# Kernel tuning notes

Hardware: AMD Instinct MI355X
Metric: run time of the kernel (lower is better)

## Reference

```python
import jax, jax.numpy as jnp
import numpy as np

EPS_BN = 1e-5
EPS_LN = 1e-5

def _bn(x, g, b, m, v):
    # inference-mode BatchNorm2d over channel dim 1
    scale = g / jnp.sqrt(v + EPS_BN)
    return x * scale[None, :, None, None] + (b - m * scale)[None, :, None, None]

def _conv1x1(x, w, b=None):
    y = jnp.einsum('bchw,oc->bohw', x, w)
    if b is not None:
        y = y + b[None, :, None, None]
    return y

def _gelu(x):
    return jax.nn.gelu(x, approximate=False)

def setup_inputs() -> dict:
    key = jax.random.key(0)
    ks = jax.random.split(key, 40)
    B, C, H, W = 32, 160, 56, 56
    C5, C3 = C // 5, C * 3
    s = 0.05
    d = {}
    d['x'] = jax.random.normal(ks[0], (B, C, H, W), jnp.float32)
    d['bn1_g'] = jax.random.uniform(ks[1], (C,), jnp.float32, 0.5, 1.5)
    d['bn1_b'] = jax.random.normal(ks[2], (C,)) * s
    d['bn1_m'] = jax.random.normal(ks[3], (C,)) * s
    d['bn1_v'] = jnp.ones((C,), jnp.float32)
    names = ['t', 'b', 'r', 'l', 'c']
    for i, n in enumerate(names):
        d['w' + n] = jax.random.normal(ks[4 + i], (C5, C)) * s
        d['b' + n] = jax.random.normal(ks[9 + i], (C5,)) * s
    d['wf1'] = jax.random.normal(ks[14], (C, C)) * s
    d['bf1'] = jax.random.normal(ks[15], (C,)) * s
    d['bn2_g'] = jax.random.uniform(ks[16], (C,), jnp.float32, 0.5, 1.5)
    d['bn2_b'] = jax.random.normal(ks[17], (C,)) * s
    d['bn2_m'] = jax.random.normal(ks[18], (C,)) * s
    d['bn2_v'] = jnp.ones((C,), jnp.float32)
    d['wph'] = jax.random.normal(ks[19], (W, W)) * s
    d['bph'] = jax.random.normal(ks[20], (W,)) * s
    d['wpw'] = jax.random.normal(ks[21], (H, H)) * s
    d['bpw'] = jax.random.normal(ks[22], (H,)) * s
    d['wf2'] = jax.random.normal(ks[23], (C, C3)) * s
    d['ln_g'] = jax.random.uniform(ks[24], (C,), jnp.float32, 0.5, 1.5)
    d['ln_b'] = jax.random.normal(ks[25], (C,)) * s
    d['wfc1'] = jax.random.normal(ks[26], (C3, C)) * s
    d['bfc1'] = jax.random.normal(ks[27], (C3,)) * s
    d['wfc2'] = jax.random.normal(ks[28], (C, C3)) * s
    d['bfc2'] = jax.random.normal(ks[29], (C,)) * s
    d['step'] = 1
    return d

def reference(x, bn1_g, bn1_b, bn1_m, bn1_v, wt, bt, wb, bb, wr, br, wl, bl, wc, bc,
              wf1, bf1, bn2_g, bn2_b, bn2_m, bn2_v, wph, bph, wpw, bpw, wf2,
              ln_g, ln_b, wfc1, bfc1, wfc2, bfc2, step):
    B, C, H, W = x.shape
    # ---- localMix: ShiftedPillarsConcatentation_BNAct_NP5 ----
    h = _gelu(_bn(x, bn1_g, bn1_b, bn1_m, bn1_v))
    x_t = _conv1x1(h, wt, bt)
    x_b = _conv1x1(h, wb, bb)
    x_r = _conv1x1(h, wr, br)
    x_l = _conv1x1(h, wl, bl)
    x_c = _conv1x1(h, wc, bc)
    # pad then narrow exactly as torch: t/l shift by 1, b/r shift by step
    x_t = jnp.pad(x_t, ((0, 0), (0, 0), (0, step), (0, 0)))[:, :, 1:1 + H, :]
    x_b = jnp.pad(x_b, ((0, 0), (0, 0), (step, 0), (0, 0)))[:, :, 0:H, :]
    x_l = jnp.pad(x_l, ((0, 0), (0, 0), (0, 0), (0, step)))[:, :, :, 1:1 + W]
    x_r = jnp.pad(x_r, ((0, 0), (0, 0), (0, 0), (step, 0)))[:, :, :, 0:W]
    lm = _conv1x1(jnp.concatenate([x_t, x_b, x_r, x_l, x_c], axis=1), wf1, bf1)
    # ---- globalMix: sparseMLP_BNAct ----
    g = _gelu(_bn(lm, bn2_g, bn2_b, bn2_m, bn2_v))
    # proj_h mixes the W axis (input permuted to (B,W,C,H)), bias per output W
    x_h = jnp.einsum('bchw,vw->bchv', g, wph) + bph[None, None, None, :]
    # proj_w mixes the H axis (input permuted to (B,H,C,W)), bias per output H
    x_w = jnp.einsum('bchw,uh->bcuw', g, wpw) + bpw[None, None, :, None]
    gm = _conv1x1(jnp.concatenate([g, x_h, x_w], axis=1), wf2)  # no bias
    x1 = gm + x  # residual 1
    # ---- channelMix: LN + Mlp over channels ----
    y = jnp.transpose(x1, (0, 2, 3, 1))  # BHWC
    mu = jnp.mean(y, axis=-1, keepdims=True)
    var = jnp.mean(jnp.square(y - mu), axis=-1, keepdims=True)
    y = (y - mu) / jnp.sqrt(var + EPS_LN) * ln_g + ln_b
    y = _gelu(jnp.einsum('bhwc,fc->bhwf', y, wfc1) + bfc1)
    y = jnp.einsum('bhwf,cf->bhwc', y, wfc2) + bfc2
    return jnp.transpose(y, (0, 3, 1, 2)) + x1  # residual 2
```

## Files before the change

### kernel.cpp

```cpp
#include <hip/hip_runtime.h>
#include <hip/hip_bf16.h>
#include <math.h>

typedef __hip_bfloat16 bf16;
typedef __attribute__((ext_vector_type(8))) short s8v;
typedef __attribute__((ext_vector_type(4))) float f4v;

#define Bn  32
#define Cn  160
#define HWn 3136
#define Pn  100352

__device__ __forceinline__ float b2f(bf16 v){ return __bfloat162float(v); }
__device__ __forceinline__ bf16  f2b(float v){ return __float2bfloat16(v); }
__device__ __forceinline__ float bits2f(unsigned short u){
    union { float f; unsigned int i; } x; x.i = ((unsigned int)u) << 16; return x.f;
}
__device__ __forceinline__ float gelu_f(float x){ return 0.5f*x*(1.0f + erff(x*0.7071067811865476f)); }

#define MFMA(a,b,c) __builtin_amdgcn_mfma_f32_16x16x32_bf16((a),(b),(c),0,0,0)

__global__ __launch_bounds__(256) void k0_prep(
    const float* __restrict__ wt, const float* __restrict__ wb_, const float* __restrict__ wr,
    const float* __restrict__ wl, const float* __restrict__ wc,
    const float* __restrict__ bt, const float* __restrict__ bb_, const float* __restrict__ br,
    const float* __restrict__ bl, const float* __restrict__ bc,
    const float* __restrict__ wf1, const float* __restrict__ bf1,
    const float* __restrict__ g2, const float* __restrict__ b2, const float* __restrict__ m2, const float* __restrict__ v2,
    const float* __restrict__ wf2, const float* __restrict__ wfc1, const float* __restrict__ wfc2,
    const float* __restrict__ wph, const float* __restrict__ wpw,
    bf16* wcat, bf16* wf1b, bf16* wf2b, bf16* wfc1b, bf16* wfc2b, bf16* wphb, bf16* wpwb,
    float* bcat, float* epsv, float* eptv)
{
    int idx = blockIdx.x*256 + threadIdx.x;
    if (idx < 25600){ int o = idx/160, k = idx - o*160; int gi = o>>5, oo = o&31;
        const float* wp = gi==0?wt: gi==1?wb_: gi==2?wr: gi==3?wl: wc;
        wcat[idx] = f2b(wp[oo*160+k]); return; }
    idx -= 25600;
    if (idx < 25600){ wf1b[idx] = f2b(wf1[idx]); return; }
    idx -= 25600;
    if (idx < 76800){ wf2b[idx] = f2b(wf2[idx]); return; }
    idx -= 76800;
    if (idx < 76800){ wfc1b[idx] = f2b(wfc1[idx]); return; }
    idx -= 76800;
    if (idx < 76800){ wfc2b[idx] = f2b(wfc2[idx]); return; }
    idx -= 76800;
    if (idx < 4096){ int v = idx>>6, w = idx&63;
        wphb[idx] = (v<56 && w<56) ? f2b(wph[v*56+w]) : f2b(0.f); return; }
    idx -= 4096;
    if (idx < 4096){ int v = idx>>6, w = idx&63;
        wpwb[idx] = (v<56 && w<56) ? f2b(wpw[v*56+w]) : f2b(0.f); return; }
    idx -= 4096;
    if (idx < 160){ int o = idx; int gi = o>>5, oo = o&31;
        const float* bp = gi==0?bt: gi==1?bb_: gi==2?br: gi==3?bl: bc;
        bcat[o] = bp[oo]; return; }
    idx -= 160;
    if (idx < 160){ int o = idx; float s = g2[o]*rsqrtf(v2[o]+1e-5f);
        epsv[o] = s; eptv[o] = (bf1[o]-m2[o])*s + b2[o]; return; }
}

__global__ __launch_bounds__(256) void k1_bn_gelu_tr(const float* __restrict__ x,
    const float* __restrict__ g, const float* __restrict__ b,
    const float* __restrict__ m, const float* __restrict__ v,
    bf16* __restrict__ hT)
{
    __shared__ float tile[64*161];
    __shared__ float sc[160], sh[160];
    int blk = blockIdx.x; int bb = blk/49; int hw0 = (blk - bb*49)*64;
    int tid = threadIdx.x;
    if (tid < 160){
        float s = g[tid] * rsqrtf(v[tid] + 1e-5f);
        sc[tid] = s; sh[tid] = b[tid] - m[tid]*s;
    }
    __syncthreads();
    const float* xb = x + (size_t)bb*Cn*HWn + hw0;
    for (int idx = tid; idx < 160*64; idx += 256){
        int c = idx >> 6, p = idx & 63;
        float val = xb[(size_t)c*HWn + p];
        tile[p*161 + c] = gelu_f(val*sc[c] + sh[c]);
    }
    __syncthreads();
    bf16* ho = hT + ((size_t)bb*HWn + hw0)*Cn;
    for (int idx = tid; idx < 64*160; idx += 256){
        int p = idx/160, c = idx - p*160;
        ho[idx] = f2b(tile[p*161 + c]);
    }
}

__global__ __launch_bounds__(256) void k2_conv5(const bf16* __restrict__ hT,
    const bf16* __restrict__ wcat, const float* __restrict__ bcat, bf16* __restrict__ y5T)
{
    __shared__ __align__(16) unsigned short Bs[2][16*168];
    int tid = threadIdx.x, wave = tid>>6, lane = tid&63, m = lane&15, q = lane>>4;
    size_t pos0 = (size_t)blockIdx.x*64;
    const unsigned short* Ap = (const unsigned short*)hT + (pos0 + wave*16 + m)*160 + q*8;
    s8v a[5];
    #pragma unroll
    for (int kb = 0; kb < 5; ++kb) a[kb] = *(const s8v*)(Ap + kb*32);
    { const s8v* sp = (const s8v*)((const unsigned short*)wcat);
      for (int c = tid; c < 320; c += 256){ int row = c/20, col = (c - row*20)*8;
          *(s8v*)&Bs[0][row*168 + col] = sp[c]; } }
    __syncthreads();
    for (int s = 0; s < 10; ++s){
        if (s+1 < 10){
            const s8v* sp = (const s8v*)((const unsigned short*)wcat + (size_t)(s+1)*2560);
            for (int c = tid; c < 320; c += 256){ int row = c/20, col = (c - row*20)*8;
                *(s8v*)&Bs[(s+1)&1][row*168 + col] = sp[c]; }
        }
        f4v acc = {0.f,0.f,0.f,0.f};
        const unsigned short* Bp = &Bs[s&1][m*168 + q*8];
        #pragma unroll
        for (int kb = 0; kb < 5; ++kb) acc = MFMA(a[kb], *(const s8v*)(Bp + kb*32), acc);
        float bias = bcat[s*16 + m];
        bf16* yo = y5T + (pos0 + wave*16 + q*4)*160 + s*16 + m;
        #pragma unroll
        for (int r = 0; r < 4; ++r) yo[r*160] = f2b(acc[r] + bias);
        __syncthreads();
    }
}

__global__ __launch_bounds__(256) void k3_wf1(const bf16* __restrict__ y5T,
    const bf16* __restrict__ wf1b, const float* __restrict__ epsv, const float* __restrict__ eptv,
    bf16* __restrict__ gT)
{
    __shared__ __align__(16) unsigned short Bs[2][16*168];
    int tid = threadIdx.x, wave = tid>>6, lane = tid&63, m = lane&15, q = lane>>4;
    int blk = blockIdx.x; int bb = blk/49; int hw0 = (blk - bb*49)*64;
    size_t pos0 = (size_t)bb*HWn + hw0;
    int phw = hw0 + wave*16 + m; int h = phw/56, w = phw - h*56;
    s8v a[5];
    #pragma unroll
    for (int kb = 0; kb < 5; ++kb){
        int h2 = h, w2 = w; bool ok = true;
        if      (kb == 0){ h2 = h+1; ok = (h2 < 56); }
        else if (kb == 1){ h2 = h-1; ok = (h2 >= 0); }
        else if (kb == 2){ w2 = w-1; ok = (w2 >= 0); }
        else if (kb == 3){ w2 = w+1; ok = (w2 < 56); }
        if (ok){
            const unsigned short* Ap = (const unsigned short*)y5T +
                ((size_t)bb*HWn + h2*56 + w2)*160 + kb*32 + q*8;
            a[kb] = *(const s8v*)Ap;
        } else {
            a[kb] = (s8v){0,0,0,0,0,0,0,0};
        }
    }
    { const s8v* sp = (const s8v*)((const unsigned short*)wf1b);
      for (int c = tid; c < 320; c += 256){ int row = c/20, col = (c - row*20)*8;
          *(s8v*)&Bs[0][row*168 + col] = sp[c]; } }
    __syncthreads();
    for (int s = 0; s < 10; ++s){
        if (s+1 < 10){
            const s8v* sp = (const s8v*)((const unsigned short*)wf1b + (size_t)(s+1)*2560);
            for (int c = tid; c < 320; c += 256){ int row = c/20, col = (c - row*20)*8;
                *(s8v*)&Bs[(s+1)&1][row*168 + col] = sp[c]; }
        }
        f4v acc = {0.f,0.f,0.f,0.f};
        const unsigned short* Bp = &Bs[s&1][m*168 + q*8];
        #pragma unroll
        for (int kb = 0; kb < 5; ++kb) acc = MFMA(a[kb], *(const s8v*)(Bp + kb*32), acc);
        int o = s*16 + m;
        float es = epsv[o], et = eptv[o];
        bf16* go = gT + (pos0 + wave*16 + q*4)*160 + o;
        #pragma unroll
        for (int r = 0; r < 4; ++r) go[r*160] = f2b(gelu_f(acc[r]*es + et));
        __syncthreads();
    }
}

__global__ __launch_bounds__(256) void k4_projh(const bf16* __restrict__ gT,
    const bf16* __restrict__ wphb, const float* __restrict__ bph, bf16* __restrict__ xhT)
{
    __shared__ __align__(16) unsigned short gS[160*72];
    int tid = threadIdx.x, wave = tid>>6, lane = tid&63, m = lane&15, q = lane>>4;
    int blk = blockIdx.x; int b = blk/56, h = blk - b*56;
    const unsigned short* ga = (const unsigned short*)gT + ((size_t)b*HWn + h*56)*160;
    for (int idx = tid; idx < 56*160; idx += 256){
        int w = idx/160, c = idx - w*160;
        gS[c*72 + w] = ga[idx];
    }
    for (int idx = tid; idx < 160*8; idx += 256){
        int c = idx>>3, w = 56 + (idx&7);
        gS[c*72 + w] = 0;
    }
    __syncthreads();
    int v0 = wave*16;
    s8v a[2];
    #pragma unroll
    for (int kb = 0; kb < 2; ++kb)
        a[kb] = *(const s8v*)((const unsigned short*)wphb + (v0+m)*64 + kb*32 + q*8);
    int v = v0 + q*4;
    for (int s = 0; s < 10; ++s){
        f4v acc = {0.f,0.f,0.f,0.f};
        const unsigned short* Bp = &gS[(s*16+m)*72 + q*8];
        #pragma unroll
        for (int kb = 0; kb < 2; ++kb) acc = MFMA(a[kb], *(const s8v*)(Bp + kb*32), acc);
        #pragma unroll
        for (int r = 0; r < 4; ++r){
            int vv = v + r;
            if (vv < 56)
                xhT[((size_t)b*HWn + h*56 + vv)*160 + s*16 + m] = f2b(acc[r] + bph[vv]);
        }
    }
}

__global__ __launch_bounds__(256) void k5_projw(const bf16* __restrict__ gT,
    const bf16* __restrict__ wpwb, const float* __restrict__ bpw, bf16* __restrict__ xwT)
{
    __shared__ __align__(16) unsigned short gS[160*72];
    int tid = threadIdx.x, wave = tid>>6, lane = tid&63, m = lane&15, q = lane>>4;
    int blk = blockIdx.x; int b = blk/56, w = blk - b*56;
    const unsigned short* gbase = (const unsigned short*)gT + ((size_t)b*HWn + w)*160;
    for (int idx = tid; idx < 56*160; idx += 256){
        int hh = idx/160, c = idx - hh*160;
        gS[c*72 + hh] = gbase[(size_t)hh*56*160 + c];
    }
    for (int idx = tid; idx < 160*8; idx += 256){
        int c = idx>>3, hh = 56 + (idx&7);
        gS[c*72 + hh] = 0;
    }
    __syncthreads();
    int v0 = wave*16;
    s8v a[2];
    #pragma unroll
    for (int kb = 0; kb < 2; ++kb)
        a[kb] = *(const s8v*)((const unsigned short*)wpwb + (v0+m)*64 + kb*32 + q*8);
    int v = v0 + q*4;
    for (int s = 0; s < 10; ++s){
        f4v acc = {0.f,0.f,0.f,0.f};
        const unsigned short* Bp = &gS[(s*16+m)*72 + q*8];
        #pragma unroll
        for (int kb = 0; kb < 2; ++kb) acc = MFMA(a[kb], *(const s8v*)(Bp + kb*32), acc);
        #pragma unroll
        for (int r = 0; r < 4; ++r){
            int vv = v + r;
            if (vv < 56)
                xwT[((size_t)b*HWn + vv*56 + w)*160 + s*16 + m] = f2b(acc[r] + bpw[vv]);
        }
    }
}

__global__ __launch_bounds__(256) void k6_wf2(const bf16* __restrict__ gT,
    const bf16* __restrict__ xhT, const bf16* __restrict__ xwT,
    const bf16* __restrict__ wf2b, bf16* __restrict__ gm)
{
    __shared__ __align__(16) unsigned short Bs[2][16*488];
    int tid = threadIdx.x, wave = tid>>6, lane = tid&63, m = lane&15, q = lane>>4;
    size_t pos0 = (size_t)blockIdx.x*64;
    size_t prow = (pos0 + wave*16 + m)*160;
    s8v a[15];
    #pragma unroll
    for (int kb = 0; kb < 15; ++kb){
        const bf16* src = (kb < 5) ? gT : (kb < 10 ? xhT : xwT);
        int kc = (kb - (kb < 5 ? 0 : (kb < 10 ? 5 : 10)))*32 + q*8;
        a[kb] = *(const s8v*)((const unsigned short*)src + prow + kc);
    }
    { const s8v* sp = (const s8v*)((const unsigned short*)wf2b);
      for (int c = tid; c < 960; c += 256){ int row = c/60, col = (c - row*60)*8;
          *(s8v*)&Bs[0][row*488 + col] = sp[c]; } }
    __syncthreads();
    for (int s = 0; s < 10; ++s){
        if (s+1 < 10){
            const s8v* sp = (const s8v*)((const unsigned short*)wf2b + (size_t)(s+1)*7680);
            for (int c = tid; c < 960; c += 256){ int row = c/60, col = (c - row*60)*8;
                *(s8v*)&Bs[(s+1)&1][row*488 + col] = sp[c]; }
        }
        f4v acc = {0.f,0.f,0.f,0.f};
        const unsigned short* Bp = &Bs[s&1][m*488 + q*8];
        #pragma unroll
        for (int kb = 0; kb < 15; ++kb) acc = MFMA(a[kb], *(const s8v*)(Bp + kb*32), acc);
        bf16* go = gm + (pos0 + wave*16 + q*4)*160 + s*16 + m;
        #pragma unroll
        for (int r = 0; r < 4; ++r) go[r*160] = f2b(acc[r]);
        __syncthreads();
    }
}

__global__ __launch_bounds__(256) void k7_ln_fc1(const float* __restrict__ x,
    const bf16* __restrict__ gm,
    const float* __restrict__ lng, const float* __restrict__ lnb,
    const bf16* __restrict__ wfc1b, const float* __restrict__ bfc1, bf16* __restrict__ u)
{
    __shared__ float Xs[64*161];
    __shared__ __align__(16) unsigned short As[64*168];
    __shared__ __align__(16) unsigned short Bs[2][16*168];
    int tid = threadIdx.x, wave = tid>>6, lane = tid&63, m = lane&15, q = lane>>4;
    int blk = blockIdx.x; int bb = blk/49; int hw0 = (blk - bb*49)*64;
    size_t pos0 = (size_t)bb*HWn + hw0;
    const float* xb = x + (size_t)bb*Cn*HWn + hw0;
    for (int idx = tid; idx < 160*64; idx += 256){
        int o = idx >> 6, p = idx & 63;
        Xs[p*161 + o] = xb[(size_t)o*HWn + p];
    }
    { const s8v* sp = (const s8v*)((const unsigned short*)wfc1b);
      for (int c = tid; c < 320; c += 256){ int row = c/20, col = (c - row*20)*8;
          *(s8v*)&Bs[0][row*168 + col] = sp[c]; } }
    __syncthreads();
    {
        int p = tid >> 2, q4 = tid & 3;
        const unsigned short* gp = (const unsigned short*)gm + (pos0 + p)*160 + q4*40;
        float s = 0.f, ss = 0.f;
        #pragma unroll 8
        for (int i = 0; i < 40; ++i){
            int c = q4*40 + i;
            float vv = Xs[p*161 + c] + bits2f(gp[i]);
            Xs[p*161 + c] = vv;
            s += vv; ss += vv*vv;
        }
        s  += __shfl_xor(s, 1);  ss += __shfl_xor(ss, 1);
        s  += __shfl_xor(s, 2);  ss += __shfl_xor(ss, 2);
        float mean = s * (1.f/160.f);
        float var  = ss * (1.f/160.f) - mean*mean;
        float rstd = rsqrtf(var + 1e-5f);
        #pragma unroll 8
        for (int i = 0; i < 40; ++i){
            int c = q4*40 + i;
            float nv = (Xs[p*161 + c] - mean)*rstd*lng[c] + lnb[c];
            union { unsigned short us; bf16 b; } cv; cv.b = f2b(nv);
            As[p*168 + c] = cv.us;
        }
    }
    __syncthreads();
    s8v a[5];
    const unsigned short* Ap = &As[(wave*16 + m)*168 + q*8];
    #pragma unroll
    for (int kb = 0; kb < 5; ++kb) a[kb] = *(const s8v*)(Ap + kb*32);
    for (int s = 0; s < 30; ++s){
        if (s+1 < 30){
            const s8v* sp = (const s8v*)((const unsigned short*)wfc1b + (size_t)(s+1)*2560);
            for (int c = tid; c < 320; c += 256){ int row = c/20, col = (c - row*20)*8;
                *(s8v*)&Bs[(s+1)&1][row*168 + col] = sp[c]; }
        }
        f4v acc = {0.f,0.f,0.f,0.f};
        const unsigned short* Bp = &Bs[s&1][m*168 + q*8];
        #pragma unroll
        for (int kb = 0; kb < 5; ++kb) acc = MFMA(a[kb], *(const s8v*)(Bp + kb*32), acc);
        float bias = bfc1[s*16 + m];
        bf16* uo = u + (pos0 + wave*16 + q*4)*480 + s*16 + m;
        #pragma unroll
        for (int r = 0; r < 4; ++r) uo[r*480] = f2b(gelu_f(acc[r] + bias));
        __syncthreads();
    }
}

__global__ __launch_bounds__(256) void k8_fc2(const bf16* __restrict__ u,
    const bf16* __restrict__ wfc2b, const float* __restrict__ bfc2,
    const float* __restrict__ x, const bf16* __restrict__ gm, float* __restrict__ out)
{
    __shared__ float Ds[64*161];
    __shared__ __align__(16) unsigned short Bs[2][16*488];
    int tid = threadIdx.x, wave = tid>>6, lane = tid&63, m = lane&15, q = lane>>4;
    int blk = blockIdx.x; int bb = blk/49; int hw0 = (blk - bb*49)*64;
    size_t pos0 = (size_t)bb*HWn + hw0;
    const float* xb = x + (size_t)bb*Cn*HWn + hw0;
    for (int idx = tid; idx < 160*64; idx += 256){
        int o = idx >> 6, p = idx & 63;
        Ds[p*161 + o] = xb[(size_t)o*HWn + p];
    }
    { const s8v* sp = (const s8v*)((const unsigned short*)wfc2b);
      for (int c = tid; c < 960; c += 256){ int row = c/60, col = (c - row*60)*8;
          *(s8v*)&Bs[0][row*488 + col] = sp[c]; } }
    __syncthreads();
    {
        const unsigned short* gp = (const unsigned short*)gm + pos0*160;
        for (int idx = tid; idx < 64*160; idx += 256){
            int p = idx/160, c = idx - p*160;
            Ds[p*161 + c] += bits2f(gp[idx]);
        }
    }
    __syncthreads();
    const unsigned short* Ap = (const unsigned short*)u + (pos0 + wave*16 + m)*480 + q*8;
    s8v a[15];
    #pragma unroll
    for (int kb = 0; kb < 15; ++kb) a[kb] = *(const s8v*)(Ap + kb*32);
    for (int s = 0; s < 10; ++s){
        if (s+1 < 10){
            const s8v* sp = (const s8v*)((const unsigned short*)wfc2b + (size_t)(s+1)*7680);
            for (int c = tid; c < 960; c += 256){ int row = c/60, col = (c - row*60)*8;
                *(s8v*)&Bs[(s+1)&1][row*488 + col] = sp[c]; }
        }
        f4v acc = {0.f,0.f,0.f,0.f};
        const unsigned short* Bp = &Bs[s&1][m*488 + q*8];
        #pragma unroll
        for (int kb = 0; kb < 15; ++kb) acc = MFMA(a[kb], *(const s8v*)(Bp + kb*32), acc);
        int o = s*16 + m; float bias = bfc2[o];
        #pragma unroll
        for (int r = 0; r < 4; ++r)
            Ds[(wave*16 + q*4 + r)*161 + o] += acc[r] + bias;
        __syncthreads();
    }
    float* ob = out + (size_t)bb*Cn*HWn + hw0;
    for (int idx = tid; idx < 160*64; idx += 256){
        int o = idx >> 6, p = idx & 63;
        ob[(size_t)o*HWn + p] = Ds[p*161 + o];
    }
}

extern "C" void kernel_launch(void* const* d_in, const int* in_sizes, int n_in,
                              void* d_out, int out_size, void* d_ws, size_t ws_size,
                              hipStream_t stream)
{
    (void)in_sizes; (void)n_in; (void)out_size; (void)ws_size;
    const float* x     = (const float*)d_in[0];
    const float* bn1g  = (const float*)d_in[1];
    const float* bn1b  = (const float*)d_in[2];
    const float* bn1m  = (const float*)d_in[3];
    const float* bn1v  = (const float*)d_in[4];
    const float* wt    = (const float*)d_in[5];
    const float* bt    = (const float*)d_in[6];
    const float* wb    = (const float*)d_in[7];
    const float* bb    = (const float*)d_in[8];
    const float* wr    = (const float*)d_in[9];
    const float* br    = (const float*)d_in[10];
    const float* wl    = (const float*)d_in[11];
    const float* bl    = (const float*)d_in[12];
    const float* wc    = (const float*)d_in[13];
    const float* bc    = (const float*)d_in[14];
    const float* wf1   = (const float*)d_in[15];
    const float* bf1   = (const float*)d_in[16];
    const float* bn2g  = (const float*)d_in[17];
    const float* bn2b  = (const float*)d_in[18];
    const float* bn2m  = (const float*)d_in[19];
    const float* bn2v  = (const float*)d_in[20];
    const float* wph   = (const float*)d_in[21];
    const float* bph   = (const float*)d_in[22];
    const float* wpw   = (const float*)d_in[23];
    const float* bpw   = (const float*)d_in[24];
    const float* wf2   = (const float*)d_in[25];
    const float* lng   = (const float*)d_in[26];
    const float* lnb   = (const float*)d_in[27];
    const float* wfc1  = (const float*)d_in[28];
    const float* bfc1  = (const float*)d_in[29];
    const float* wfc2  = (const float*)d_in[30];
    const float* bfc2v = (const float*)d_in[31];
    float* outp = (float*)d_out;

    const size_t PC2 = (size_t)Pn*160*2;
    char* ws = (char*)d_ws;
    bf16* hT   = (bf16*)(ws + 0*PC2);
    bf16* y5T  = (bf16*)(ws + 1*PC2);
    bf16* gT   = (bf16*)(ws + 2*PC2);
    bf16* xhT  = (bf16*)(ws + 3*PC2);
    bf16* xwT  = (bf16*)(ws + 4*PC2);
    bf16* gm   = (bf16*)(ws + 5*PC2);
    char* wsw  = ws + 6*PC2;
    bf16*  wcat  = (bf16*)(wsw + 0);
    bf16*  wf1b  = (bf16*)(wsw + 51200);
    bf16*  wf2b  = (bf16*)(wsw + 102400);
    bf16*  wfc1b = (bf16*)(wsw + 256000);
    bf16*  wfc2b = (bf16*)(wsw + 409600);
    bf16*  wphb  = (bf16*)(wsw + 563200);
    bf16*  wpwb  = (bf16*)(wsw + 571392);
    float* bcat  = (float*)(wsw + 579584);
    float* epsv  = (float*)(wsw + 580224);
    float* eptv  = (float*)(wsw + 580864);
    bf16* uB   = (bf16*)(ws + 0);

    const int GP = Pn/64;
    const int GS = Bn*56;

    k0_prep<<<1134, 256, 0, stream>>>(wt, wb, wr, wl, wc, bt, bb, br, bl, bc,
                                      wf1, bf1, bn2g, bn2b, bn2m, bn2v,
                                      wf2, wfc1, wfc2, wph, wpw,
                                      wcat, wf1b, wf2b, wfc1b, wfc2b, wphb, wpwb,
                                      bcat, epsv, eptv);
    k1_bn_gelu_tr<<<GP, 256, 0, stream>>>(x, bn1g, bn1b, bn1m, bn1v, hT);
    k2_conv5     <<<GP, 256, 0, stream>>>(hT, wcat, bcat, y5T);
    k3_wf1       <<<GP, 256, 0, stream>>>(y5T, wf1b, epsv, eptv, gT);
    k4_projh     <<<GS, 256, 0, stream>>>(gT, wphb, bph, xhT);
    k5_projw     <<<GS, 256, 0, stream>>>(gT, wpwb, bpw, xwT);
    k6_wf2       <<<GP, 256, 0, stream>>>(gT, xhT, xwT, wf2b, gm);
    k7_ln_fc1    <<<GP, 256, 0, stream>>>(x, gm, lng, lnb, wfc1b, bfc1, uB);
    k8_fc2       <<<GP, 256, 0, stream>>>(uB, wfc2b, bfc2v, x, gm, outp);
}
```

Before: 559.5 us.

## Fold LayerNorm affine into fc1 weights and stream B operands from registers

LayerNorm gamma is folded into the fc1 weights, and beta plus the bias are folded into precomputed per-output vectors in the prep kernel. The fc1 GEMM now runs on the raw residual sum (x+gm) in bf16, and per-row mean and rstd are applied after the MFMA. B-fragments are loaded directly from global memory into registers with double buffering, which removes the shared-memory B staging and the per-step __syncthreads. The smaller shared-memory footprint (aliased X/A buffer) allows launch_bounds(256,4) for higher occupancy, at the risk of larger bf16 error because non-centred values are quantised before normalisation.

```diff
diff --git a/kernel.cpp b/kernel.cpp
--- a/kernel.cpp
+++ b/kernel.cpp
@@ -29,8 +29,9 @@
     const float* __restrict__ g2, const float* __restrict__ b2, const float* __restrict__ m2, const float* __restrict__ v2,
     const float* __restrict__ wf2, const float* __restrict__ wfc1, const float* __restrict__ wfc2,
     const float* __restrict__ wph, const float* __restrict__ wpw,
-    bf16* wcat, bf16* wf1b, bf16* wf2b, bf16* wfc1b, bf16* wfc2b, bf16* wphb, bf16* wpwb,
-    float* bcat, float* epsv, float* eptv)
+    const float* __restrict__ lng, const float* __restrict__ lnb, const float* __restrict__ bfc1,
+    bf16* wcat, bf16* wf1b, bf16* wf2b, bf16* wfc1g, bf16* wfc2b, bf16* wphb, bf16* wpwb,
+    float* bcat, float* epsv, float* eptv, float* wgs, float* wcb)
 {
     int idx = blockIdx.x*256 + threadIdx.x;
     if (idx < 25600){ int o = idx/160, k = idx - o*160; int gi = o>>5, oo = o&31;
@@ -41,7 +42,8 @@
     idx -= 25600;
     if (idx < 76800){ wf2b[idx] = f2b(wf2[idx]); return; }
     idx -= 76800;
-    if (idx < 76800){ wfc1b[idx] = f2b(wfc1[idx]); return; }
+    if (idx < 76800){ int f = idx/160, c = idx - f*160;
+        wfc1g[idx] = f2b(wfc1[f*160+c] * lng[c]); return; }
     idx -= 76800;
     if (idx < 76800){ wfc2b[idx] = f2b(wfc2[idx]); return; }
     idx -= 76800;
@@ -57,6 +59,11 @@
     idx -= 160;
     if (idx < 160){ int o = idx; float s = g2[o]*rsqrtf(v2[o]+1e-5f);
         epsv[o] = s; eptv[o] = (bf1[o]-m2[o])*s + b2[o]; return; }
+    idx -= 160;
+    if (idx < 480){ int o = idx; float sg = 0.f, sb = 0.f;
+        const float* wr_ = wfc1 + (size_t)o*160;
+        for (int c = 0; c < 160; ++c){ float w = wr_[c]; sg += w*lng[c]; sb += w*lnb[c]; }
+        wgs[o] = sg; wcb[o] = sb + bfc1[o]; return; }
 }
 
 __global__ __launch_bounds__(256) void k1_bn_gelu_tr(const float* __restrict__ x,
@@ -275,70 +282,106 @@
     }
 }
 
-__global__ __launch_bounds__(256) void k7_ln_fc1(const float* __restrict__ x,
+__global__ __launch_bounds__(256,4) void k7_ln_fc1(const float* __restrict__ x,
     const bf16* __restrict__ gm,
-    const float* __restrict__ lng, const float* __restrict__ lnb,
-    const bf16* __restrict__ wfc1b, const float* __restrict__ bfc1, bf16* __restrict__ u)
-{
-    __shared__ float Xs[64*161];
-    __shared__ __align__(16) unsigned short As[64*168];
-    __shared__ __align__(16) unsigned short Bs[2][16*168];
+    const bf16* __restrict__ wfc1g, const float* __restrict__ wgs, const float* __restrict__ wcb,
+    bf16* __restrict__ u)
+{
+    __shared__ __align__(16) float XsU[160*64];
+    unsigned short* As = (unsigned short*)XsU;
+    float* rstd_s = XsU + 5120;
+    float* mrs_s  = XsU + 5184;
     int tid = threadIdx.x, wave = tid>>6, lane = tid&63, m = lane&15, q = lane>>4;
     int blk = blockIdx.x; int bb = blk/49; int hw0 = (blk - bb*49)*64;
     size_t pos0 = (size_t)bb*HWn + hw0;
     const float* xb = x + (size_t)bb*Cn*HWn + hw0;
     for (int idx = tid; idx < 160*64; idx += 256){
-        int o = idx >> 6, p = idx & 63;
-        Xs[p*161 + o] = xb[(size_t)o*HWn + p];
-    }
-    { const s8v* sp = (const s8v*)((const unsigned short*)wfc1b);
-      for (int c = tid; c < 320; c += 256){ int row = c/20, col = (c - row*20)*8;
-          *(s8v*)&Bs[0][row*168 + col] = sp[c]; } }
-    __syncthreads();
+        int c = idx >> 6, p = idx & 63;
+        XsU[idx] = xb[(size_t)c*HWn + p];
+    }
+    __syncthreads();
+    int p = tid >> 2, q4 = tid & 3;
     {
-        int p = tid >> 2, q4 = tid & 3;
-        const unsigned short* gp = (const unsigned short*)gm + (pos0 + p)*160 + q4*40;
+        const s8v* gp = (const s8v*)((const unsigned short*)gm + (pos0 + p)*160 + q4*40);
+        float y[40];
         float s = 0.f, ss = 0.f;
-        #pragma unroll 8
-        for (int i = 0; i < 40; ++i){
-            int c = q4*40 + i;
-            float vv = Xs[p*161 + c] + bits2f(gp[i]);
-            Xs[p*161 + c] = vv;
-            s += vv; ss += vv*vv;
+        #pragma unroll
+        for (int j = 0; j < 5; ++j){
+            s8v gv = gp[j];
+            #pragma unroll
+            for (int t = 0; t < 8; ++t){
+                int i = j*8 + t;
+                float vv = XsU[(q4*40 + i)*64 + p] + bits2f((unsigned short)gv[t]);
+                y[i] = vv; s += vv; ss += vv*vv;
+            }
         }
         s  += __shfl_xor(s, 1);  ss += __shfl_xor(ss, 1);
         s  += __shfl_xor(s, 2);  ss += __shfl_xor(ss, 2);
         float mean = s * (1.f/160.f);
         float var  = ss * (1.f/160.f) - mean*mean;
         float rstd = rsqrtf(var + 1e-5f);
-        #pragma unroll 8
-        for (int i = 0; i < 40; ++i){
-            int c = q4*40 + i;
-            float nv = (Xs[p*161 + c] - mean)*rstd*lng[c] + lnb[c];
-            union { unsigned short us; bf16 b; } cv; cv.b = f2b(nv);
-            As[p*168 + c] = cv.us;
-        }
+        __syncthreads();
+        #pragma unroll
+        for (int j = 0; j < 5; ++j){
+            s8v pk;
+            #pragma unroll
+            for (int t = 0; t < 8; ++t){
+                union { unsigned short us; bf16 b; } cv; cv.b = f2b(y[j*8 + t]);
+                pk[t] = (short)cv.us;
+            }
+            *(s8v*)&As[p*160 + q4*40 + j*8] = pk;
+        }
+        if (q4 == 0){ rstd_s[p] = rstd; mrs_s[p] = -mean*rstd; }
     }
     __syncthreads();
     s8v a[5];
-    const unsigned short* Ap = &As[(wave*16 + m)*168 + q*8];
+    const unsigned short* Ap = &As[(wave*16 + m)*160 + q*8];
     #pragma unroll
     for (int kb = 0; kb < 5; ++kb) a[kb] = *(const s8v*)(Ap + kb*32);
-    for (int s = 0; s < 30; ++s){
-        if (s+1 < 30){
-            const s8v* sp = (const s8v*)((const unsigned short*)wfc1b + (size_t)(s+1)*2560);
-            for (int c = tid; c < 320; c += 256){ int row = c/20, col = (c - row*20)*8;
-                *(s8v*)&Bs[(s+1)&1][row*168 + col] = sp[c]; }
-        }
-        f4v acc = {0.f,0.f,0.f,0.f};
-        const unsigned short* Bp = &Bs[s&1][m*168 + q*8];
-        #pragma unroll
-        for (int kb = 0; kb < 5; ++kb) acc = MFMA(a[kb], *(const s8v*)(Bp + kb*32), acc);
-        float bias = bfc1[s*16 + m];
-        bf16* uo = u + (pos0 + wave*16 + q*4)*480 + s*16 + m;
-        #pragma unroll
-        for (int r = 0; r < 4; ++r) uo[r*480] = f2b(gelu_f(acc[r] + bias));
-        __syncthreads();
+    float rst[4], mrs[4];
+    #pragma unroll
+    for (int r = 0; r < 4; ++r){
+        rst[r] = rstd_s[wave*16 + q*4 + r];
+        mrs[r] = mrs_s [wave*16 + q*4 + r];
+    }
+    const unsigned short* Wp = (const unsigned short*)wfc1g + (size_t)m*160 + q*8;
+    bf16* uo = u + (pos0 + wave*16 + q*4)*480 + m;
+    s8v b0[5], b1[5];
+    #pragma unroll
+    for (int kb = 0; kb < 5; ++kb) b0[kb] = *(const s8v*)(Wp + kb*32);
+    for (int s = 0; s < 30; s += 2){
+        {
+            const unsigned short* Wn = Wp + (size_t)(s+1)*2560;
+            #pragma unroll
+            for (int kb = 0; kb < 5; ++kb) b1[kb] = *(const s8v*)(Wn + kb*32);
+        }
+        f4v acc = {0.f,0.f,0.f,0.f};
+        #pragma unroll
+        for (int kb = 0; kb < 5; ++kb) acc = MFMA(a[kb], b0[kb], acc);
+        {
+            int o = s*16 + m; float wg = wgs[o], wc = wcb[o];
+            #pragma unroll
+            for (int r = 0; r < 4; ++r){
+                float v = acc[r]*rst[r] + mrs[r]*wg + wc;
+                uo[(size_t)r*480 + s*16] = f2b(gelu_f(v));
+            }
+        }
+        if (s + 2 < 30){
+            const unsigned short* Wn = Wp + (size_t)(s+2)*2560;
+            #pragma unroll
+            for (int kb = 0; kb < 5; ++kb) b0[kb] = *(const s8v*)(Wn + kb*32);
+        }
+        f4v acc2 = {0.f,0.f,0.f,0.f};
+        #pragma unroll
+        for (int kb = 0; kb < 5; ++kb) acc2 = MFMA(a[kb], b1[kb], acc2);
+        {
+            int o = (s+1)*16 + m; float wg = wgs[o], wc = wcb[o];
+            #pragma unroll
+            for (int r = 0; r < 4; ++r){
+                float v = acc2[r]*rst[r] + mrs[r]*wg + wc;
+                uo[(size_t)r*480 + (s+1)*16] = f2b(gelu_f(v));
+            }
+        }
     }
 }
 
@@ -446,29 +489,32 @@
     bf16*  wcat  = (bf16*)(wsw + 0);
     bf16*  wf1b  = (bf16*)(wsw + 51200);
     bf16*  wf2b  = (bf16*)(wsw + 102400);
-    bf16*  wfc1b = (bf16*)(wsw + 256000);
+    bf16*  wfc1g = (bf16*)(wsw + 256000);
     bf16*  wfc2b = (bf16*)(wsw + 409600);
     bf16*  wphb  = (bf16*)(wsw + 563200);
     bf16*  wpwb  = (bf16*)(wsw + 571392);
     float* bcat  = (float*)(wsw + 579584);
     float* epsv  = (float*)(wsw + 580224);
     float* eptv  = (float*)(wsw + 580864);
+    float* wgs   = (float*)(wsw + 581504);
+    float* wcb   = (float*)(wsw + 583424);
     bf16* uB   = (bf16*)(ws + 0);
 
     const int GP = Pn/64;
     const int GS = Bn*56;
 
-    k0_prep<<<1134, 256, 0, stream>>>(wt, wb, wr, wl, wc, bt, bb, br, bl, bc,
+    k0_prep<<<1136, 256, 0, stream>>>(wt, wb, wr, wl, wc, bt, bb, br, bl, bc,
                                       wf1, bf1, bn2g, bn2b, bn2m, bn2v,
                                       wf2, wfc1, wfc2, wph, wpw,
-                                      wcat, wf1b, wf2b, wfc1b, wfc2b, wphb, wpwb,
-                                      bcat, epsv, eptv);
+                                      lng, lnb, bfc1,
+                                      wcat, wf1b, wf2b, wfc1g, wfc2b, wphb, wpwb,
+                                      bcat, epsv, eptv, wgs, wcb);
     k1_bn_gelu_tr<<<GP, 256, 0, stream>>>(x, bn1g, bn1b, bn1m, bn1v, hT);
     k2_conv5     <<<GP, 256, 0, stream>>>(hT, wcat, bcat, y5T);
     k3_wf1       <<<GP, 256, 0, stream>>>(y5T, wf1b, epsv, eptv, gT);
     k4_projh     <<<GS, 256, 0, stream>>>(gT, wphb, bph, xhT);
     k5_projw     <<<GS, 256, 0, stream>>>(gT, wpwb, bpw, xwT);
     k6_wf2       <<<GP, 256, 0, stream>>>(gT, xhT, xwT, wf2b, gm);
-    k7_ln_fc1    <<<GP, 256, 0, stream>>>(x, gm, lng, lnb, wfc1b, bfc1, uB);
+    k7_ln_fc1    <<<GP, 256, 0, stream>>>(x, gm, wfc1g, wgs, wcb, uB);
     k8_fc2       <<<GP, 256, 0, stream>>>(uB, wfc2b, bfc2v, x, gm, outp);
 }
```

Result: faster. 506.6 us (-9.5%).
